# Optimization experiments

Hardware: AMD Instinct MI355X
Metric: run time of the kernel (lower is better)

Reference implementation:

```python
import jax, jax.numpy as jnp
import numpy as np

B, S, E, H, L, FF = 32, 256, 768, 12, 2, 2048
DH = E // H
N_HIST, N_TGT = 128, 127  # fixed layout: pos0=type0, 1..128=type1 (hist), 129..255=type2 (target)
HIST_MASK_RATIO, MASK_RATIO, TAU = 0.5, 0.5, 1.0
KEEP_HIST = max(1, int(N_HIST * (1.0 - HIST_MASK_RATIO)))  # 64
KEEP_TGT = max(1, int(N_TGT * (1.0 - MASK_RATIO)))        # 63
INFERENCE = False
EPS = 1e-5
NEG = -1e30


def _sinusoidal_pe():
    pos = np.arange(257, dtype=np.float32)[:, None]
    div = np.exp(np.arange(0, E, 2, dtype=np.float32) * (-np.log(10000.0) / E))
    pe = np.zeros((257, E), np.float32)
    pe[:, 0::2] = np.sin(pos * div)
    pe[:, 1::2] = np.cos(pos * div)
    return jnp.asarray(pe)


def setup_inputs() -> dict:
    key = jax.random.key(0)
    ks = jax.random.split(key, 12)
    rn = lambda k, sh, s=1.0: jax.random.normal(k, sh, dtype=jnp.float32) * s
    inp = {}
    inp['token_embeds'] = rn(ks[0], (B, S, E))
    inp['attention_mask'] = jnp.zeros((B, S), dtype=bool)  # no padding
    inp['position_ids'] = jnp.tile(jnp.arange(S, dtype=jnp.int32), (B, 1))
    row = jnp.concatenate([jnp.zeros((1,), jnp.int32), jnp.ones((N_HIST,), jnp.int32), jnp.full((N_TGT,), 2, jnp.int32)])
    inp['type_ids'] = jnp.tile(row, (B, 1))
    inp['gumbel_hist'] = jax.random.gumbel(ks[1], (B, S), dtype=jnp.float32)
    inp['gumbel_target'] = jax.random.gumbel(ks[2], (B, S), dtype=jnp.float32)
    inp['pe'] = _sinusoidal_pe()
    inp['type_emb'] = rn(ks[3], (3, E), 0.02)
    inp['ln_w'] = jnp.ones((E,), jnp.float32); inp['ln_b'] = jnp.zeros((E,), jnp.float32)
    inp['dense_w'] = rn(ks[4], (E, E), 0.02); inp['dense_b'] = jnp.zeros((E,), jnp.float32)
    inp['qkv_w'] = rn(ks[5], (L, 3 * E, E), 0.02); inp['qkv_b'] = jnp.zeros((L, 3 * E), jnp.float32)
    inp['out_w'] = rn(ks[6], (L, E, E), 0.02); inp['out_b'] = jnp.zeros((L, E), jnp.float32)
    inp['ln1_w'] = jnp.ones((L, E), jnp.float32); inp['ln1_b'] = jnp.zeros((L, E), jnp.float32)
    inp['lin1_w'] = rn(ks[7], (L, FF, E), 0.02); inp['lin1_b'] = jnp.zeros((L, FF), jnp.float32)
    inp['lin2_w'] = rn(ks[8], (L, E, FF), 0.02); inp['lin2_b'] = jnp.zeros((L, E), jnp.float32)
    inp['ln2_w'] = jnp.ones((L, E), jnp.float32); inp['ln2_b'] = jnp.zeros((L, E), jnp.float32)
    return inp


def _ln(x, w, b):
    m = x.mean(-1, keepdims=True)
    v = jnp.mean((x - m) ** 2, -1, keepdims=True)
    return (x - m) * jax.lax.rsqrt(v + EPS) * w + b


def _masked_softmax(score, m):
    e = jnp.exp(score) * m
    return e / jnp.sum(e, -1, keepdims=True)


def _gumbel_topk(prob, valid, gumbel, keep_num):
    vm = valid.astype(prob.dtype)
    logits = jnp.where(valid, jnp.log(jnp.where(valid, prob, 1.0)), NEG)
    gl = jnp.where(valid, (logits + gumbel) / TAU, NEG)
    y_soft = jax.nn.softmax(gl, axis=-1)  # invalid positions get exactly 0
    idx = jax.lax.top_k(y_soft, keep_num)[1]
    y_hard = jnp.zeros_like(y_soft).at[jnp.arange(B)[:, None], idx].set(1.0)
    return (y_hard - jax.lax.stop_gradient(y_soft) + y_soft) * vm


def reference(token_embeds, attention_mask, position_ids, type_ids, gumbel_hist, gumbel_target,
              pe, type_emb, ln_w, ln_b, dense_w, dense_b, qkv_w, qkv_b, out_w, out_b,
              ln1_w, ln1_b, lin1_w, lin1_b, lin2_w, lin2_b, ln2_w, ln2_b):
    # get_input_embeds (dropout = identity in eval)
    x = _ln(token_embeds + pe[position_ids] + type_emb[type_ids], ln_w, ln_b)
    # TransformerEncoder (post-norm, relu FFN, key_padding_mask)
    kpm = attention_mask[:, None, None, :]
    for l in range(L):
        qkv = x @ qkv_w[l].T + qkv_b[l]
        q, k, v = jnp.split(qkv, 3, axis=-1)
        q = q.reshape(B, S, H, DH); k = k.reshape(B, S, H, DH); v = v.reshape(B, S, H, DH)
        sc = jnp.einsum('bqhd,bkhd->bhqk', q, k) / np.float32(np.sqrt(DH))
        sc = jnp.where(kpm, NEG, sc)
        o = jnp.einsum('bhqk,bkhd->bqhd', jax.nn.softmax(sc, -1), v).reshape(B, S, E)
        x = _ln(x + o @ out_w[l].T + out_b[l], ln1_w[l], ln1_b[l])
        f = jax.nn.relu(x @ lin1_w[l].T + lin1_b[l]) @ lin2_w[l].T + lin2_b[l]
        x = _ln(x + f, ln2_w[l], ln2_b[l])
    out = _ln(x, ln_w, ln_b)
    out = jnp.tanh(out @ dense_w.T + dense_b)
    # cosine similarity (torch eps=1e-8)
    na = jnp.linalg.norm(token_embeds, axis=-1)
    nb = jnp.linalg.norm(out, axis=-1)
    cos = jnp.sum(token_embeds * out, -1) / jnp.maximum(na * nb, 1e-8)
    hist_mask = type_ids == 1
    tgt_mask = type_ids == 2
    hp = _masked_softmax(cos, hist_mask.astype(cos.dtype))
    tp0 = _masked_softmax(cos, tgt_mask.astype(cos.dtype))
    tp = tp0 if INFERENCE else 1.0 - tp0
    hist_ret = _gumbel_topk(hp, hist_mask, gumbel_hist, KEEP_HIST)
    tgt_ret = _gumbel_topk(tp, tgt_mask, gumbel_target, KEEP_TGT)
    return hist_ret + tgt_ret
```

## Files before the change

### kernel.cpp

```cpp
#include <hip/hip_runtime.h>
#include <math.h>

#define B_ 32
#define S_ 256
#define E_ 768
#define H_ 12
#define L_ 2
#define FF_ 2048
#define NEGV -1e30f

typedef __attribute__((ext_vector_type(8))) short bf16x8;
typedef __attribute__((ext_vector_type(4))) float f32x4;

__device__ __forceinline__ short bf16_rne(float x) {
  unsigned u = __float_as_uint(x);
  u += 0x7fffu + ((u >> 16) & 1u);
  return (short)(u >> 16);
}
__device__ __forceinline__ float bf16_to_f32(short h) {
  return __uint_as_float(((unsigned)(unsigned short)h) << 16);
}
__device__ __forceinline__ void split_bf16(float v, short& h, short& l) {
  h = bf16_rne(v);
  l = bf16_rne(v - bf16_to_f32(h));
}

__device__ __forceinline__ void gl2lds16(const short* g, short* s) {
  __builtin_amdgcn_global_load_lds((const __attribute__((address_space(1))) void*)g,
                                   (__attribute__((address_space(3))) void*)s, 16, 0, 0);
}

__device__ __forceinline__ float block_sum256(float v) {
  __shared__ float sh[4];
  int lane = threadIdx.x & 63, w = threadIdx.x >> 6;
#pragma unroll
  for (int off = 32; off; off >>= 1) v += __shfl_down(v, off);
  if (lane == 0) sh[w] = v;
  __syncthreads();
  float tot = sh[0] + sh[1] + sh[2] + sh[3];
  __syncthreads();
  return tot;
}

__global__ __launch_bounds__(256) void embed_ln_kernel(
    const float* __restrict__ tok, const int* __restrict__ pos,
    const int* __restrict__ typ, const float* __restrict__ pe,
    const float* __restrict__ temb, const float* __restrict__ w,
    const float* __restrict__ b, float* __restrict__ out,
    short* __restrict__ ohi, short* __restrict__ olo) {
  int row = blockIdx.x;
  int t = threadIdx.x;
  int p = pos[row], ty = typ[row];
  const float* tr = tok + (size_t)row * E_;
  const float* pr = pe + (size_t)p * E_;
  const float* yr = temb + (size_t)ty * E_;
  float v0 = tr[t] + pr[t] + yr[t];
  float v1 = tr[t + 256] + pr[t + 256] + yr[t + 256];
  float v2 = tr[t + 512] + pr[t + 512] + yr[t + 512];
  float m = block_sum256(v0 + v1 + v2) * (1.f / E_);
  float d0 = v0 - m, d1 = v1 - m, d2 = v2 - m;
  float var = block_sum256(d0 * d0 + d1 * d1 + d2 * d2) * (1.f / E_);
  float rs = 1.f / sqrtf(var + 1e-5f);
  size_t base = (size_t)row * E_;
  float r0 = d0 * rs * w[t] + b[t];
  float r1 = d1 * rs * w[t + 256] + b[t + 256];
  float r2 = d2 * rs * w[t + 512] + b[t + 512];
  out[base + t] = r0; out[base + t + 256] = r1; out[base + t + 512] = r2;
  short h, l;
  split_bf16(r0, h, l); ohi[base + t] = h; olo[base + t] = l;
  split_bf16(r1, h, l); ohi[base + t + 256] = h; olo[base + t + 256] = l;
  split_bf16(r2, h, l); ohi[base + t + 512] = h; olo[base + t + 512] = l;
}

__global__ __launch_bounds__(256) void ln_kernel(
    const float* __restrict__ in, const float* __restrict__ w,
    const float* __restrict__ b, float* __restrict__ out,
    short* __restrict__ ohi, short* __restrict__ olo) {
  int row = blockIdx.x;
  int t = threadIdx.x;
  const float* p = in + (size_t)row * E_;
  float v0 = p[t], v1 = p[t + 256], v2 = p[t + 512];
  float m = block_sum256(v0 + v1 + v2) * (1.f / E_);
  float d0 = v0 - m, d1 = v1 - m, d2 = v2 - m;
  float var = block_sum256(d0 * d0 + d1 * d1 + d2 * d2) * (1.f / E_);
  float rs = 1.f / sqrtf(var + 1e-5f);
  size_t base = (size_t)row * E_;
  float r0 = d0 * rs * w[t] + b[t];
  float r1 = d1 * rs * w[t + 256] + b[t + 256];
  float r2 = d2 * rs * w[t + 512] + b[t + 512];
  if (out) {
    out[base + t] = r0; out[base + t + 256] = r1; out[base + t + 512] = r2;
  }
  short h, l;
  split_bf16(r0, h, l); ohi[base + t] = h; olo[base + t] = l;
  split_bf16(r1, h, l); ohi[base + t + 256] = h; olo[base + t + 256] = l;
  split_bf16(r2, h, l); ohi[base + t + 512] = h; olo[base + t + 512] = l;
}

__global__ __launch_bounds__(256) void split_kernel(
    const float* __restrict__ src, short* __restrict__ hi,
    short* __restrict__ lo, int n4) {
  int i = blockIdx.x * 256 + threadIdx.x;
  if (i >= n4) return;
  float4 v = ((const float4*)src)[i];
  short4 h, l;
  split_bf16(v.x, h.x, l.x);
  split_bf16(v.y, h.y, l.y);
  split_bf16(v.z, h.z, l.z);
  split_bf16(v.w, h.w, l.w);
  ((short4*)hi)[i] = h;
  ((short4*)lo)[i] = l;
}

template <int BN_, int WM_, int WN_, int ACT, int RES, int OSPLIT>
__global__ __launch_bounds__(512, 2) void gemm_big(
    const short* __restrict__ Ahi, const short* __restrict__ Alo,
    const short* __restrict__ Whi, const short* __restrict__ Wlo,
    const float* __restrict__ bias, const float* __restrict__ Rres,
    float* __restrict__ Cf, short* __restrict__ Chi, short* __restrict__ Clo,
    int M, int N, int K, int nx, int cpx) {
  constexpr int BM_ = 256;
  constexpr int MR = WM_ / 16, NR = WN_ / 16;
  constexpr int NWC = BN_ / WN_;
  constexpr int CHUNKS = 2 * BM_ + 2 * BN_;
  constexpr int OPS_FULL = CHUNKS / 128;
  constexpr int REM = CHUNKS - OPS_FULL * 128;
  constexpr int BUFSH = CHUNKS * 32;

  __shared__ short lds[2 * BUFSH];
  const int t = threadIdx.x;
  const int l = t & 63;
  const int w = t >> 6;
  const int wr = w / NWC, wc = w % NWC;
  const int li = l & 15, lh = l >> 4;

  int id = blockIdx.x;
  int id2 = (id & 7) * cpx + (id >> 3);
  const int n0 = (id2 % nx) * BN_, m0 = (id2 / nx) * BM_;

  const int cks = t & 3;
  auto mksrc = [&](int c) -> const short* {
    const short* base; int row;
    if (c < BM_) { base = Ahi; row = m0 + c; }
    else if (c < 2 * BM_) { base = Alo; row = m0 + c - BM_; }
    else if (c < 2 * BM_ + BN_) { base = Whi; row = n0 + c - 2 * BM_; }
    else { base = Wlo; row = n0 + c - 2 * BM_ - BN_; }
    return base + (size_t)row * K + (cks ^ ((c >> 1) & 3)) * 8;
  };
  const short* sp[OPS_FULL + 1];
#pragma unroll
  for (int o = 0; o < OPS_FULL; ++o) sp[o] = mksrc(o * 128 + (t >> 2));
  if (REM) sp[OPS_FULL] = mksrc((t < 256) ? (OPS_FULL * 128 + (t >> 2)) : 0);

  auto stage = [&](int buf, int k0) {
    short* base = lds + buf * BUFSH;
#pragma unroll
    for (int o = 0; o < OPS_FULL; ++o)
      gl2lds16(sp[o] + k0, base + o * 4096 + w * 512);
    if (REM) {
      if (t < 256)
        gl2lds16(sp[OPS_FULL] + k0, base + OPS_FULL * 4096 + w * 512);
    }
  };

  const int kb_r = (lh ^ ((l >> 1) & 3)) * 8;

  float bv[NR];
#pragma unroll
  for (int ni = 0; ni < NR; ++ni) bv[ni] = bias[n0 + wc * WN_ + ni * 16 + li];

  f32x4 acc[MR][NR] = {};
  const int ns = K >> 5;

  stage(0, 0);

  for (int s = 0; s < ns; ++s) {
    const int bp = s & 1;
    __builtin_amdgcn_s_barrier();
    if (s + 1 < ns) {
      stage(bp ^ 1, (s + 1) * 32);
      __builtin_amdgcn_sched_barrier(0);
      if (REM) {
        if (w < 4)
          asm volatile("s_waitcnt vmcnt(%0)" ::"n"(OPS_FULL + 1) : "memory");
        else
          asm volatile("s_waitcnt vmcnt(%0)" ::"n"(OPS_FULL) : "memory");
      } else {
        asm volatile("s_waitcnt vmcnt(%0)" ::"n"(OPS_FULL) : "memory");
      }
    } else {
      __builtin_amdgcn_sched_barrier(0);
      asm volatile("s_waitcnt vmcnt(0)" ::: "memory");
    }
    __builtin_amdgcn_s_barrier();

    const short* bufp = lds + bp * BUFSH;
    bf16x8 ah[MR], al[MR];
#pragma unroll
    for (int mi = 0; mi < MR; ++mi) {
      int row = wr * WM_ + mi * 16 + li;
      ah[mi] = *(const bf16x8*)(bufp + row * 32 + kb_r);
      al[mi] = *(const bf16x8*)(bufp + BM_ * 32 + row * 32 + kb_r);
    }
    __builtin_amdgcn_s_setprio(1);
#pragma unroll
    for (int ni = 0; ni < NR; ++ni) {
      int rowB = wc * WN_ + ni * 16 + li;
      bf16x8 bh = *(const bf16x8*)(bufp + 2 * BM_ * 32 + rowB * 32 + kb_r);
      bf16x8 bl = *(const bf16x8*)(bufp + (2 * BM_ + BN_) * 32 + rowB * 32 + kb_r);
#pragma unroll
      for (int mi = 0; mi < MR; ++mi) {
        acc[mi][ni] = __builtin_amdgcn_mfma_f32_16x16x32_bf16(ah[mi], bh, acc[mi][ni], 0, 0, 0);
        acc[mi][ni] = __builtin_amdgcn_mfma_f32_16x16x32_bf16(ah[mi], bl, acc[mi][ni], 0, 0, 0);
        acc[mi][ni] = __builtin_amdgcn_mfma_f32_16x16x32_bf16(al[mi], bh, acc[mi][ni], 0, 0, 0);
      }
    }
    __builtin_amdgcn_s_setprio(0);
  }

  const int col_l = l & 15;
  const int row_l = (l >> 4) * 4;
#pragma unroll
  for (int mi = 0; mi < MR; ++mi) {
#pragma unroll
    for (int ni = 0; ni < NR; ++ni) {
      int col = n0 + wc * WN_ + ni * 16 + col_l;
      float bvv = bv[ni];
#pragma unroll
      for (int r = 0; r < 4; ++r) {
        int row = m0 + wr * WM_ + mi * 16 + row_l + r;
        float v = acc[mi][ni][r] + bvv;
        if (RES) v += Rres[(size_t)row * N + col];
        if (ACT == 1) v = fmaxf(v, 0.f);
        if (ACT == 2) v = tanhf(v);
        if (OSPLIT) {
          short h2, l2;
          split_bf16(v, h2, l2);
          Chi[(size_t)row * N + col] = h2;
          Clo[(size_t)row * N + col] = l2;
        } else {
          Cf[(size_t)row * N + col] = v;
        }
      }
    }
  }
}

__global__ __launch_bounds__(256, 2) void attn_kernel(
    const float* __restrict__ qkv, short* __restrict__ t1h,
    short* __restrict__ t1l) {
  __shared__ short lds[16384];
  const int qt = blockIdx.x, h = blockIdx.y, b = blockIdx.z;
  const int t = threadIdx.x;
  const int w = t >> 6, l = t & 63;
  const int li = l & 15, lh = l >> 4;

  short* kh = lds;
  short* kl = lds + 4096;
  short* ph = lds + 8192 + w * 2048;
  short* pl = ph + 1024;

  const int tok0 = b * S_ + qt * 64;

  bf16x8 qh[2], ql[2];
  {
    const float* qrow = qkv + (size_t)(tok0 + w * 16 + li) * 2304 + h * 64 + lh * 8;
#pragma unroll
    for (int s = 0; s < 2; s++) {
      float4 f0 = *(const float4*)(qrow + s * 32);
      float4 f1 = *(const float4*)(qrow + s * 32 + 4);
      float f[8] = {f0.x, f0.y, f0.z, f0.w, f1.x, f1.y, f1.z, f1.w};
      bf16x8 hv, lv;
#pragma unroll
      for (int j = 0; j < 8; j++) {
        short hs, ls2;
        split_bf16(f[j], hs, ls2);
        hv[j] = hs; lv[j] = ls2;
      }
      qh[s] = hv; ql[s] = lv;
    }
  }

  const int skk = t >> 2, sd0 = (t & 3) * 16;

  f32x4 acc[16] = {};

  const float* kbase = qkv + (size_t)(b * S_) * 2304 + 768 + h * 64;
#pragma unroll
  for (int c = 0; c < 4; c++) {
    __syncthreads();
    {
      const float* src = kbase + (size_t)(c * 64 + skk) * 2304 + sd0;
#pragma unroll
      for (int i = 0; i < 4; i++) {
        float4 f = *(const float4*)(src + i * 4);
        int d = sd0 + i * 4;
        short4 hv, lv;
        split_bf16(f.x, hv.x, lv.x);
        split_bf16(f.y, hv.y, lv.y);
        split_bf16(f.z, hv.z, lv.z);
        split_bf16(f.w, hv.w, lv.w);
        int off = skk * 64 + ((((d >> 3) ^ (skk & 7)) & 7) << 3) + (d & 7);
        *(short4*)(kh + off) = hv;
        *(short4*)(kl + off) = lv;
      }
    }
    __syncthreads();
#pragma unroll
    for (int nn = 0; nn < 4; nn++) {
      const int krow = nn * 16 + li;
#pragma unroll
      for (int s = 0; s < 2; s++) {
        const int off = krow * 64 + ((((s * 4 + lh) ^ (li & 7)) & 7) << 3);
        bf16x8 bh = *(const bf16x8*)(kh + off);
        bf16x8 bl = *(const bf16x8*)(kl + off);
        acc[c * 4 + nn] = __builtin_amdgcn_mfma_f32_16x16x32_bf16(qh[s], bh, acc[c * 4 + nn], 0, 0, 0);
        acc[c * 4 + nn] = __builtin_amdgcn_mfma_f32_16x16x32_bf16(qh[s], bl, acc[c * 4 + nn], 0, 0, 0);
        acc[c * 4 + nn] = __builtin_amdgcn_mfma_f32_16x16x32_bf16(ql[s], bh, acc[c * 4 + nn], 0, 0, 0);
      }
    }
  }

  float rs_[4];
#pragma unroll
  for (int r = 0; r < 4; r++) {
    float m = -3.4e38f;
#pragma unroll
    for (int fi = 0; fi < 16; fi++) m = fmaxf(m, acc[fi][r]);
#pragma unroll
    for (int off = 8; off; off >>= 1) m = fmaxf(m, __shfl_xor(m, off));
    float sum = 0.f;
#pragma unroll
    for (int fi = 0; fi < 16; fi++) {
      float p = expf((acc[fi][r] - m) * 0.125f);
      acc[fi][r] = p;
      sum += p;
    }
#pragma unroll
    for (int off = 8; off; off >>= 1) sum += __shfl_xor(sum, off);
    rs_[r] = sum;
  }

  f32x4 oacc[4] = {};
  const float* vbase = qkv + (size_t)(b * S_) * 2304 + 1536 + h * 64;
#pragma unroll
  for (int c = 0; c < 4; c++) {
    __syncthreads();
    {
      const float* src = vbase + (size_t)(c * 64 + skk) * 2304 + sd0;
#pragma unroll
      for (int i = 0; i < 4; i++) {
        float4 f = *(const float4*)(src + i * 4);
        float fv[4] = {f.x, f.y, f.z, f.w};
#pragma unroll
        for (int j = 0; j < 4; j++) {
          int d = sd0 + i * 4 + j;
          short hs, ls2;
          split_bf16(fv[j], hs, ls2);
          int sw = (d & 7) ^ ((d >> 3) & 7);
          int off = d * 64 + ((((skk >> 3) ^ sw) & 7) << 3) + (skk & 7);
          kh[off] = hs;
          kl[off] = ls2;
        }
      }
    }
#pragma unroll
    for (int nn = 0; nn < 4; nn++) {
#pragma unroll
      for (int r = 0; r < 4; r++) {
        const int q = lh * 4 + r;
        const int keyl = li + 16 * nn;
        short hs, ls2;
        split_bf16(acc[c * 4 + nn][r], hs, ls2);
        const int off = q * 64 + ((((keyl >> 3) ^ (q & 7)) & 7) << 3) + (keyl & 7);
        ph[off] = hs;
        pl[off] = ls2;
      }
    }
    __syncthreads();
    bf16x8 pah[2], pal[2];
#pragma unroll
    for (int s = 0; s < 2; s++) {
      const int off = li * 64 + ((((s * 4 + lh) ^ (li & 7)) & 7) << 3);
      pah[s] = *(const bf16x8*)(ph + off);
      pal[s] = *(const bf16x8*)(pl + off);
    }
#pragma unroll
    for (int dn = 0; dn < 4; dn++) {
      const int drow = dn * 16 + li;
      const int sw = ((drow & 7) ^ ((drow >> 3) & 7)) & 7;
#pragma unroll
      for (int s = 0; s < 2; s++) {
        const int off = drow * 64 + ((((s * 4 + lh) ^ sw) & 7) << 3);
        bf16x8 vh = *(const bf16x8*)(kh + off);
        bf16x8 vl = *(const bf16x8*)(kl + off);
        oacc[dn] = __builtin_amdgcn_mfma_f32_16x16x32_bf16(pah[s], vh, oacc[dn], 0, 0, 0);
        oacc[dn] = __builtin_amdgcn_mfma_f32_16x16x32_bf16(pah[s], vl, oacc[dn], 0, 0, 0);
        oacc[dn] = __builtin_amdgcn_mfma_f32_16x16x32_bf16(pal[s], vh, oacc[dn], 0, 0, 0);
      }
    }
  }

  float rinv[4];
#pragma unroll
  for (int r = 0; r < 4; r++) rinv[r] = 1.f / rs_[r];
#pragma unroll
  for (int dn = 0; dn < 4; dn++) {
#pragma unroll
    for (int r = 0; r < 4; r++) {
      float v = oacc[dn][r] * rinv[r];
      short hs, ls2;
      split_bf16(v, hs, ls2);
      size_t oidx = (size_t)(tok0 + w * 16 + lh * 4 + r) * E_ + h * 64 + dn * 16 + li;
      t1h[oidx] = hs;
      t1l[oidx] = ls2;
    }
  }
}

__global__ __launch_bounds__(256) void cos_kernel(
    const float* __restrict__ a, const float* __restrict__ o,
    float* __restrict__ cosv) {
  int row = blockIdx.x;
  int t = threadIdx.x;
  const float* ar = a + (size_t)row * E_;
  const float* orr = o + (size_t)row * E_;
  float d = 0.f, na = 0.f, nb = 0.f;
#pragma unroll
  for (int j = 0; j < 3; j++) {
    float av = ar[t + 256 * j], ov = orr[t + 256 * j];
    d = fmaf(av, ov, d);
    na = fmaf(av, av, na);
    nb = fmaf(ov, ov, nb);
  }
  d = block_sum256(d);
  na = block_sum256(na);
  nb = block_sum256(nb);
  if (t == 0) cosv[row] = d / fmaxf(sqrtf(na) * sqrtf(nb), 1e-8f);
}

__global__ __launch_bounds__(256) void select_kernel(
    const float* __restrict__ cosv, const int* __restrict__ typ,
    const float* __restrict__ gh, const float* __restrict__ gt,
    float* __restrict__ out) {
  __shared__ float vals[256];
  int b = blockIdx.x, t = threadIdx.x;
  int idx = b * 256 + t;
  int ty = typ[idx];
  float c = cosv[idx];
  float res = 0.f;

  float eh = (ty == 1) ? expf(c) : 0.f;
  float sh = block_sum256(eh);
  float glh = (ty == 1) ? (logf(eh / sh) + gh[idx]) : NEGV;
  vals[t] = glh;
  __syncthreads();
  {
    int rank = 0;
#pragma unroll
    for (int j = 0; j < 64; ++j) {
      float4 q = *(const float4*)&vals[j * 4];
      rank += (q.x > glh) || (q.x == glh && (j * 4 + 0) < t);
      rank += (q.y > glh) || (q.y == glh && (j * 4 + 1) < t);
      rank += (q.z > glh) || (q.z == glh && (j * 4 + 2) < t);
      rank += (q.w > glh) || (q.w == glh && (j * 4 + 3) < t);
    }
    if (ty == 1 && rank < 64) res += 1.f;
  }
  __syncthreads();

  float et = (ty == 2) ? expf(c) : 0.f;
  float st = block_sum256(et);
  float glt = (ty == 2) ? (logf(1.f - et / st) + gt[idx]) : NEGV;
  vals[t] = glt;
  __syncthreads();
  {
    int rank = 0;
#pragma unroll
    for (int j = 0; j < 64; ++j) {
      float4 q = *(const float4*)&vals[j * 4];
      rank += (q.x > glt) || (q.x == glt && (j * 4 + 0) < t);
      rank += (q.y > glt) || (q.y == glt && (j * 4 + 1) < t);
      rank += (q.z > glt) || (q.z == glt && (j * 4 + 2) < t);
      rank += (q.w > glt) || (q.w == glt && (j * 4 + 3) < t);
    }
    if (ty == 2 && rank < 63) res += 1.f;
  }
  out[idx] = res;
}

extern "C" void kernel_launch(void* const* d_in, const int* in_sizes, int n_in,
                              void* d_out, int out_size, void* d_ws,
                              size_t ws_size, hipStream_t stream) {
  const float* tok = (const float*)d_in[0];
  const int* pos = (const int*)d_in[2];
  const int* typ = (const int*)d_in[3];
  const float* gh = (const float*)d_in[4];
  const float* gt = (const float*)d_in[5];
  const float* pe = (const float*)d_in[6];
  const float* temb = (const float*)d_in[7];
  const float* ln_w = (const float*)d_in[8];
  const float* ln_b = (const float*)d_in[9];
  const float* dense_w = (const float*)d_in[10];
  const float* dense_b = (const float*)d_in[11];
  const float* qkv_w = (const float*)d_in[12];
  const float* qkv_b = (const float*)d_in[13];
  const float* out_w = (const float*)d_in[14];
  const float* out_b = (const float*)d_in[15];
  const float* ln1_w = (const float*)d_in[16];
  const float* ln1_b = (const float*)d_in[17];
  const float* lin1_w = (const float*)d_in[18];
  const float* lin1_b = (const float*)d_in[19];
  const float* lin2_w = (const float*)d_in[20];
  const float* lin2_b = (const float*)d_in[21];
  const float* ln2_w = (const float*)d_in[22];
  const float* ln2_b = (const float*)d_in[23];

  const int M = B_ * S_;
  const size_t NX = (size_t)M * E_;
  const size_t NQKV = (size_t)M * 3 * E_;
  const size_t NFF = (size_t)M * FF_;

  const size_t oQ = 0;
  const size_t oO = oQ + 2 * (size_t)3 * E_ * E_;
  const size_t oL1 = oO + 2 * (size_t)E_ * E_;
  const size_t oL2 = oL1 + 2 * (size_t)FF_ * E_;
  const size_t oD = oL2 + 2 * (size_t)E_ * FF_;
  const size_t WTOT = oD + (size_t)E_ * E_;

  float* ws = (float*)d_ws;
  float* x = ws;
  float* t2 = x + NX;
  float* shared = t2 + NX;
  short* x_hi = (short*)(shared + NQKV);
  short* x_lo = x_hi + NX;
  short* t1_hi = x_lo + NX;
  short* t1_lo = t1_hi + NX;
  short* w_hi = t1_lo + NX;
  short* w_lo = w_hi + WTOT;
  float* cosb = (float*)(w_lo + WTOT);

  short* big_hi = (short*)shared;
  short* big_lo = big_hi + NFF;

  {
    int n4;
    n4 = (int)(2 * 3 * E_ * E_ / 4);
    split_kernel<<<(n4 + 255) / 256, 256, 0, stream>>>(qkv_w, w_hi + oQ, w_lo + oQ, n4);
    n4 = (int)(2 * E_ * E_ / 4);
    split_kernel<<<(n4 + 255) / 256, 256, 0, stream>>>(out_w, w_hi + oO, w_lo + oO, n4);
    n4 = (int)(2 * FF_ * E_ / 4);
    split_kernel<<<(n4 + 255) / 256, 256, 0, stream>>>(lin1_w, w_hi + oL1, w_lo + oL1, n4);
    n4 = (int)(2 * E_ * FF_ / 4);
    split_kernel<<<(n4 + 255) / 256, 256, 0, stream>>>(lin2_w, w_hi + oL2, w_lo + oL2, n4);
    n4 = (int)(E_ * E_ / 4);
    split_kernel<<<(n4 + 255) / 256, 256, 0, stream>>>(dense_w, w_hi + oD, w_lo + oD, n4);
  }

  embed_ln_kernel<<<M, 256, 0, stream>>>(tok, pos, typ, pe, temb, ln_w, ln_b,
                                         x, x_hi, x_lo);

  for (int l = 0; l < L_; l++) {
    const size_t wq = oQ + (size_t)l * 3 * E_ * E_;
    const size_t wo = oO + (size_t)l * E_ * E_;
    const size_t w1 = oL1 + (size_t)l * FF_ * E_;
    const size_t w2 = oL2 + (size_t)l * E_ * FF_;
    gemm_big<288, 64, 144, 0, 0, 0><<<256, 512, 0, stream>>>(
        x_hi, x_lo, w_hi + wq, w_lo + wq, qkv_b + (size_t)l * 3 * E_, nullptr,
        shared, nullptr, nullptr, M, 3 * E_, E_, 3 * E_ / 288, 32);
    attn_kernel<<<dim3(4, H_, B_), 256, 0, stream>>>(shared, t1_hi, t1_lo);
    gemm_big<96, 64, 48, 0, 1, 0><<<256, 512, 0, stream>>>(
        t1_hi, t1_lo, w_hi + wo, w_lo + wo, out_b + (size_t)l * E_, x, t2,
        nullptr, nullptr, M, E_, E_, E_ / 96, 32);
    ln_kernel<<<M, 256, 0, stream>>>(t2, ln1_w + (size_t)l * E_,
                                     ln1_b + (size_t)l * E_, x, x_hi, x_lo);
    gemm_big<256, 128, 64, 1, 0, 1><<<256, 512, 0, stream>>>(
        x_hi, x_lo, w_hi + w1, w_lo + w1, lin1_b + (size_t)l * FF_, nullptr,
        nullptr, big_hi, big_lo, M, FF_, E_, FF_ / 256, 32);
    gemm_big<96, 64, 48, 0, 1, 0><<<256, 512, 0, stream>>>(
        big_hi, big_lo, w_hi + w2, w_lo + w2, lin2_b + (size_t)l * E_, x, t2,
        nullptr, nullptr, M, E_, FF_, E_ / 96, 32);
    ln_kernel<<<M, 256, 0, stream>>>(t2, ln2_w + (size_t)l * E_,
                                     ln2_b + (size_t)l * E_, x, x_hi, x_lo);
  }

  ln_kernel<<<M, 256, 0, stream>>>(x, ln_w, ln_b, nullptr, t1_hi, t1_lo);
  gemm_big<96, 64, 48, 2, 0, 0><<<256, 512, 0, stream>>>(
      t1_hi, t1_lo, w_hi + oD, w_lo + oD, dense_b, nullptr, shared, nullptr,
      nullptr, M, E_, E_, E_ / 96, 32);
  cos_kernel<<<M, 256, 0, stream>>>(tok, shared, cosb);
  select_kernel<<<B_, 256, 0, stream>>>(cosb, typ, gh, gt, (float*)d_out);
}
```

Measured before the change: 815.7 us.

## Interleave next-tile global-to-LDS loads with MFMA groups in three phases

In the main GEMM kernel, the prefetch of the next K-slice is split into three phases by operation index. Each phase is issued in front of one of three groups of N-subtile MFMA work, so global-to-LDS traffic is spread across the compute instead of being issued in one burst at the top of each iteration. The wait before reading the current buffer now only requires all but the newest phase-0 loads to have landed. The cost is more workgroup barriers per K-step (four instead of two), which adds synchronisation overhead and can reduce wave overlap.

Result: faster. 797.0 us, median of 2 (-2.3%).

```diff
diff --git a/kernel.cpp b/kernel.cpp
--- a/kernel.cpp
+++ b/kernel.cpp
@@ -126,6 +126,9 @@
   constexpr int OPS_FULL = CHUNKS / 128;
   constexpr int REM = CHUNKS - OPS_FULL * 128;
   constexpr int BUFSH = CHUNKS * 32;
+  constexpr int P0CNT = (OPS_FULL + 2) / 3;
+  constexpr int G0E = (NR + 2) / 3;
+  constexpr int G1E = G0E + (NR + 1) / 3;
 
   __shared__ short lds[2 * BUFSH];
   const int t = threadIdx.x;
@@ -152,12 +155,13 @@
   for (int o = 0; o < OPS_FULL; ++o) sp[o] = mksrc(o * 128 + (t >> 2));
   if (REM) sp[OPS_FULL] = mksrc((t < 256) ? (OPS_FULL * 128 + (t >> 2)) : 0);
 
-  auto stage = [&](int buf, int k0) {
+  auto stage_p = [&](int buf, int k0, int p) {
     short* base = lds + buf * BUFSH;
 #pragma unroll
     for (int o = 0; o < OPS_FULL; ++o)
-      gl2lds16(sp[o] + k0, base + o * 4096 + w * 512);
-    if (REM) {
+      if (o % 3 == p)
+        gl2lds16(sp[o] + k0, base + o * 4096 + w * 512);
+    if (REM && p == 2) {
       if (t < 256)
         gl2lds16(sp[OPS_FULL] + k0, base + OPS_FULL * 4096 + w * 512);
     }
@@ -172,30 +176,26 @@
   f32x4 acc[MR][NR] = {};
   const int ns = K >> 5;
 
-  stage(0, 0);
+  stage_p(0, 0, 0);
+  stage_p(0, 0, 1);
+  stage_p(0, 0, 2);
 
   for (int s = 0; s < ns; ++s) {
     const int bp = s & 1;
+    const bool pf = (s + 1 < ns);
+    const int k1 = (s + 1) * 32;
+    const short* bufp = lds + bp * BUFSH;
+
+    bf16x8 ah[MR], al[MR];
+
+    if (pf) stage_p(bp ^ 1, k1, 0);
+    __builtin_amdgcn_sched_barrier(0);
+    if (pf) {
+      asm volatile("s_waitcnt vmcnt(%0)" ::"n"(P0CNT) : "memory");
+    } else {
+      asm volatile("s_waitcnt vmcnt(0)" ::: "memory");
+    }
     __builtin_amdgcn_s_barrier();
-    if (s + 1 < ns) {
-      stage(bp ^ 1, (s + 1) * 32);
-      __builtin_amdgcn_sched_barrier(0);
-      if (REM) {
-        if (w < 4)
-          asm volatile("s_waitcnt vmcnt(%0)" ::"n"(OPS_FULL + 1) : "memory");
-        else
-          asm volatile("s_waitcnt vmcnt(%0)" ::"n"(OPS_FULL) : "memory");
-      } else {
-        asm volatile("s_waitcnt vmcnt(%0)" ::"n"(OPS_FULL) : "memory");
-      }
-    } else {
-      __builtin_amdgcn_sched_barrier(0);
-      asm volatile("s_waitcnt vmcnt(0)" ::: "memory");
-    }
-    __builtin_amdgcn_s_barrier();
-
-    const short* bufp = lds + bp * BUFSH;
-    bf16x8 ah[MR], al[MR];
 #pragma unroll
     for (int mi = 0; mi < MR; ++mi) {
       int row = wr * WM_ + mi * 16 + li;
@@ -204,7 +204,7 @@
     }
     __builtin_amdgcn_s_setprio(1);
 #pragma unroll
-    for (int ni = 0; ni < NR; ++ni) {
+    for (int ni = 0; ni < G0E; ++ni) {
       int rowB = wc * WN_ + ni * 16 + li;
       bf16x8 bh = *(const bf16x8*)(bufp + 2 * BM_ * 32 + rowB * 32 + kb_r);
       bf16x8 bl = *(const bf16x8*)(bufp + (2 * BM_ + BN_) * 32 + rowB * 32 + kb_r);
@@ -216,6 +216,41 @@
       }
     }
     __builtin_amdgcn_s_setprio(0);
+    __builtin_amdgcn_s_barrier();
+
+    if (pf) stage_p(bp ^ 1, k1, 1);
+    __builtin_amdgcn_s_setprio(1);
+#pragma unroll
+    for (int ni = G0E; ni < G1E; ++ni) {
+      int rowB = wc * WN_ + ni * 16 + li;
+      bf16x8 bh = *(const bf16x8*)(bufp + 2 * BM_ * 32 + rowB * 32 + kb_r);
+      bf16x8 bl = *(const bf16x8*)(bufp + (2 * BM_ + BN_) * 32 + rowB * 32 + kb_r);
+#pragma unroll
+      for (int mi = 0; mi < MR; ++mi) {
+        acc[mi][ni] = __builtin_amdgcn_mfma_f32_16x16x32_bf16(ah[mi], bh, acc[mi][ni], 0, 0, 0);
+        acc[mi][ni] = __builtin_amdgcn_mfma_f32_16x16x32_bf16(ah[mi], bl, acc[mi][ni], 0, 0, 0);
+        acc[mi][ni] = __builtin_amdgcn_mfma_f32_16x16x32_bf16(al[mi], bh, acc[mi][ni], 0, 0, 0);
+      }
+    }
+    __builtin_amdgcn_s_setprio(0);
+    __builtin_amdgcn_s_barrier();
+
+    if (pf) stage_p(bp ^ 1, k1, 2);
+    __builtin_amdgcn_s_setprio(1);
+#pragma unroll
+    for (int ni = G1E; ni < NR; ++ni) {
+      int rowB = wc * WN_ + ni * 16 + li;
+      bf16x8 bh = *(const bf16x8*)(bufp + 2 * BM_ * 32 + rowB * 32 + kb_r);
+      bf16x8 bl = *(const bf16x8*)(bufp + (2 * BM_ + BN_) * 32 + rowB * 32 + kb_r);
+#pragma unroll
+      for (int mi = 0; mi < MR; ++mi) {
+        acc[mi][ni] = __builtin_amdgcn_mfma_f32_16x16x32_bf16(ah[mi], bh, acc[mi][ni], 0, 0, 0);
+        acc[mi][ni] = __builtin_amdgcn_mfma_f32_16x16x32_bf16(ah[mi], bl, acc[mi][ni], 0, 0, 0);
+        acc[mi][ni] = __builtin_amdgcn_mfma_f32_16x16x32_bf16(al[mi], bh, acc[mi][ni], 0, 0, 0);
+      }
+    }
+    __builtin_amdgcn_s_setprio(0);
+    __builtin_amdgcn_s_barrier();
   }
 
   const int col_l = l & 15;
```

## Split GEMM k-step into three staged groups interleaving loads with MFMA

Applied to the files above, without the earlier changes.

Restructures the double-buffered GEMM main loop so each k-step's prefetch is split into three groups (A plus the first slice of B columns, then two further B slices). Each group is issued and waited on separately, and the MFMAs for the matching B columns run in between, so computation starts on partially landed data. B rows are reordered in LDS by column group to make this possible. The trade-off is three barriers per k-step instead of two, plus more complex address computation in each stage call, which may add overhead or register pressure.

New measurement: 1.697 ms, median of 2. 108% more time.

```diff
diff --git a/kernel.cpp b/kernel.cpp
--- a/kernel.cpp
+++ b/kernel.cpp
@@ -11,6 +11,9 @@
 
 typedef __attribute__((ext_vector_type(8))) short bf16x8;
 typedef __attribute__((ext_vector_type(4))) float f32x4;
+
+template <int G>
+struct IC { static constexpr int value = G; };
 
 __device__ __forceinline__ short bf16_rne(float x) {
   unsigned u = __float_as_uint(x);
@@ -122,10 +125,16 @@
   constexpr int BM_ = 256;
   constexpr int MR = WM_ / 16, NR = WN_ / 16;
   constexpr int NWC = BN_ / WN_;
-  constexpr int CHUNKS = 2 * BM_ + 2 * BN_;
-  constexpr int OPS_FULL = CHUNKS / 128;
-  constexpr int REM = CHUNKS - OPS_FULL * 128;
-  constexpr int BUFSH = CHUNKS * 32;
+  constexpr int NR0 = (NR + 2) / 3;
+  constexpr int NR12 = NR - NR0;
+  constexpr int NR1 = (NR12 + 1) / 2;
+  constexpr int NR2 = NR12 - NR1;
+  constexpr int R0 = NR0 * NWC * 16, R1 = NR1 * NWC * 16, R2 = NR2 * NWC * 16;
+  constexpr int BUFSH = (2 * BM_ + 2 * BN_) * 32;
+  constexpr int VT_LO = (2 * BM_ + 2 * R0 + 127) / 128 + (2 * R1 + 127) / 128 +
+                        (2 * R2 + 127) / 128;
+  constexpr int VT_HI = (2 * BM_ + 2 * R0) / 128 + (2 * R1) / 128 +
+                        (2 * R2) / 128;
 
   __shared__ short lds[2 * BUFSH];
   const int t = threadIdx.x;
@@ -139,31 +148,44 @@
   const int n0 = (id2 % nx) * BN_, m0 = (id2 / nx) * BM_;
 
   const int cks = t & 3;
-  auto mksrc = [&](int c) -> const short* {
-    const short* base; int row;
-    if (c < BM_) { base = Ahi; row = m0 + c; }
-    else if (c < 2 * BM_) { base = Alo; row = m0 + c - BM_; }
-    else if (c < 2 * BM_ + BN_) { base = Whi; row = n0 + c - 2 * BM_; }
-    else { base = Wlo; row = n0 + c - 2 * BM_ - BN_; }
-    return base + (size_t)row * K + (cks ^ ((c >> 1) & 3)) * 8;
+
+  auto stage_g = [&](auto GC, int buf, int k0) {
+    constexpr int g = decltype(GC)::value;
+    constexpr int GOFFg = (g == 0) ? 0 : (g == 1 ? R0 : R0 + R1);
+    constexpr int RGg = (g == 0) ? R0 : (g == 1 ? R1 : R2);
+    constexpr int CGg = (g == 0) ? (2 * BM_ + 2 * R0) : 2 * RGg;
+    constexpr int RNDg = (CGg + 127) / 128;
+    short* ldsb = lds + buf * BUFSH;
+#pragma unroll
+    for (int r = 0; r < RNDg; ++r) {
+      const int lc = r * 128 + (t >> 2);
+      if (lc < CGg) {
+        const short* base;
+        int srow, ldsrow;
+        if (g == 0 && lc < 2 * BM_) {
+          const int plane = lc >= BM_;
+          base = plane ? Alo : Ahi;
+          srow = m0 + (plane ? lc - BM_ : lc);
+          ldsrow = lc;
+        } else {
+          const int q = (g == 0) ? (lc - 2 * BM_) : lc;
+          const int plane = q >= RGg;
+          const int rowip = GOFFg + (plane ? q - RGg : q);
+          ldsrow = 2 * BM_ + plane * BN_ + rowip;
+          const int ni = rowip / (NWC * 16);
+          const int rem = rowip - ni * (NWC * 16);
+          srow = n0 + (rem >> 4) * WN_ + ni * 16 + (rem & 15);
+          base = plane ? Wlo : Whi;
+        }
+        const int kb = cks ^ ((ldsrow >> 1) & 3);
+        gl2lds16(base + (size_t)srow * K + k0 + kb * 8,
+                 ldsb + ldsrow * 32 + (t & 3) * 8);
+      }
+    }
   };
-  const short* sp[OPS_FULL + 1];
-#pragma unroll
-  for (int o = 0; o < OPS_FULL; ++o) sp[o] = mksrc(o * 128 + (t >> 2));
-  if (REM) sp[OPS_FULL] = mksrc((t < 256) ? (OPS_FULL * 128 + (t >> 2)) : 0);
-
-  auto stage = [&](int buf, int k0) {
-    short* base = lds + buf * BUFSH;
-#pragma unroll
-    for (int o = 0; o < OPS_FULL; ++o)
-      gl2lds16(sp[o] + k0, base + o * 4096 + w * 512);
-    if (REM) {
-      if (t < 256)
-        gl2lds16(sp[OPS_FULL] + k0, base + OPS_FULL * 4096 + w * 512);
-    }
-  };
 
   const int kb_r = (lh ^ ((l >> 1) & 3)) * 8;
+  const int rowBb = wc * 16 + li;
 
   float bv[NR];
 #pragma unroll
@@ -172,51 +194,66 @@
   f32x4 acc[MR][NR] = {};
   const int ns = K >> 5;
 
-  stage(0, 0);
+  stage_g(IC<0>{}, 0, 0);
+  stage_g(IC<1>{}, 0, 0);
+  stage_g(IC<2>{}, 0, 0);
+
+#define VMW()                                                        \
+  if (w < 4) { asm volatile("s_waitcnt vmcnt(%0)" ::"n"(VT_LO) : "memory"); } \
+  else { asm volatile("s_waitcnt vmcnt(%0)" ::"n"(VT_HI) : "memory"); }
+
+#define MFMA_GROUP(NI_S, NI_E)                                                  \
+  __builtin_amdgcn_s_setprio(1);                                               \
+  _Pragma("unroll") for (int ni = (NI_S); ni < (NI_E); ++ni) {                  \
+    int rowB = ni * (NWC * 16) + rowBb;                                         \
+    bf16x8 bh = *(const bf16x8*)(bufp + (2 * BM_ + rowB) * 32 + kb_r);          \
+    bf16x8 bl = *(const bf16x8*)(bufp + (2 * BM_ + BN_ + rowB) * 32 + kb_r);    \
+    _Pragma("unroll") for (int mi = 0; mi < MR; ++mi) {                         \
+      acc[mi][ni] = __builtin_amdgcn_mfma_f32_16x16x32_bf16(ah[mi], bh, acc[mi][ni], 0, 0, 0); \
+      acc[mi][ni] = __builtin_amdgcn_mfma_f32_16x16x32_bf16(ah[mi], bl, acc[mi][ni], 0, 0, 0); \
+      acc[mi][ni] = __builtin_amdgcn_mfma_f32_16x16x32_bf16(al[mi], bh, acc[mi][ni], 0, 0, 0); \
+    }                                                                           \
+  }                                                                             \
+  __builtin_amdgcn_s_setprio(0);
 
   for (int s = 0; s < ns; ++s) {
     const int bp = s & 1;
-    __builtin_amdgcn_s_barrier();
-    if (s + 1 < ns) {
-      stage(bp ^ 1, (s + 1) * 32);
-      __builtin_amdgcn_sched_barrier(0);
-      if (REM) {
-        if (w < 4)
-          asm volatile("s_waitcnt vmcnt(%0)" ::"n"(OPS_FULL + 1) : "memory");
-        else
-          asm volatile("s_waitcnt vmcnt(%0)" ::"n"(OPS_FULL) : "memory");
-      } else {
-        asm volatile("s_waitcnt vmcnt(%0)" ::"n"(OPS_FULL) : "memory");
-      }
-    } else {
-      __builtin_amdgcn_sched_barrier(0);
-      asm volatile("s_waitcnt vmcnt(0)" ::: "memory");
-    }
-    __builtin_amdgcn_s_barrier();
-
+    const bool pf = (s + 1 < ns);
+    const int k1 = (s + 1) * 32;
     const short* bufp = lds + bp * BUFSH;
     bf16x8 ah[MR], al[MR];
+
+    if (pf) stage_g(IC<0>{}, bp ^ 1, k1);
+    __builtin_amdgcn_sched_barrier(0);
+    if (pf) { VMW(); }
+    else { asm volatile("s_waitcnt vmcnt(0)" ::: "memory"); }
+    __builtin_amdgcn_s_barrier();
 #pragma unroll
     for (int mi = 0; mi < MR; ++mi) {
       int row = wr * WM_ + mi * 16 + li;
       ah[mi] = *(const bf16x8*)(bufp + row * 32 + kb_r);
       al[mi] = *(const bf16x8*)(bufp + BM_ * 32 + row * 32 + kb_r);
     }
-    __builtin_amdgcn_s_setprio(1);
-#pragma unroll
-    for (int ni = 0; ni < NR; ++ni) {
-      int rowB = wc * WN_ + ni * 16 + li;
-      bf16x8 bh = *(const bf16x8*)(bufp + 2 * BM_ * 32 + rowB * 32 + kb_r);
-      bf16x8 bl = *(const bf16x8*)(bufp + (2 * BM_ + BN_) * 32 + rowB * 32 + kb_r);
-#pragma unroll
-      for (int mi = 0; mi < MR; ++mi) {
-        acc[mi][ni] = __builtin_amdgcn_mfma_f32_16x16x32_bf16(ah[mi], bh, acc[mi][ni], 0, 0, 0);
-        acc[mi][ni] = __builtin_amdgcn_mfma_f32_16x16x32_bf16(ah[mi], bl, acc[mi][ni], 0, 0, 0);
-        acc[mi][ni] = __builtin_amdgcn_mfma_f32_16x16x32_bf16(al[mi], bh, acc[mi][ni], 0, 0, 0);
-      }
-    }
-    __builtin_amdgcn_s_setprio(0);
-  }
+    MFMA_GROUP(0, NR0)
+
+    if (pf) {
+      stage_g(IC<1>{}, bp ^ 1, k1);
+      __builtin_amdgcn_sched_barrier(0);
+      VMW();
+    }
+    __builtin_amdgcn_s_barrier();
+    MFMA_GROUP(NR0, NR0 + NR1)
+
+    if (pf) {
+      stage_g(IC<2>{}, bp ^ 1, k1);
+      __builtin_amdgcn_sched_barrier(0);
+      VMW();
+    }
+    __builtin_amdgcn_s_barrier();
+    MFMA_GROUP(NR0 + NR1, NR)
+  }
+#undef VMW
+#undef MFMA_GROUP
 
   const int col_l = l & 15;
   const int row_l = (l >> 4) * 4;
```
